# Kernel optimization log

Measured on AMD Instinct MI355X. Metric: run time of the kernel, lower is better.

The kernel has to match this reference:

```python
import jax, jax.numpy as jnp
import numpy as np
from jax import lax

B, Q, T, G = 128, 900, 256, 20
FOCAL_ALPHA, FOCAL_GAMMA = 0.25, 2.0
COEF_BBOX, COEF_GIOU, COEF_CLASS = 5.0, 2.0, 1.0
EPS = 1e-6


def setup_inputs() -> dict:
    key = jax.random.key(0)
    k1, k2, k3, k4, k5 = jax.random.split(key, 5)
    pred_logits = jax.random.normal(k1, (B, Q, T), dtype=jnp.float32)
    # pred boxes in cxcywh, valid-ish: centers in (0.2,0.8), w/h in (0.05,0.3)
    cxy_p = jax.random.uniform(k2, (B, Q, 2), minval=0.2, maxval=0.8)
    wh_p = jax.random.uniform(k3, (B, Q, 2), minval=0.05, maxval=0.3)
    pred_boxes = jnp.concatenate([cxy_p, wh_p], axis=-1).astype(jnp.float32)
    cxy_t = jax.random.uniform(k4, (B, G, 2), minval=0.2, maxval=0.8)
    wh_t = jax.random.uniform(k5, (B, G, 2), minval=0.05, maxval=0.3)
    tgt_boxes = jnp.concatenate([cxy_t, wh_t], axis=-1).astype(jnp.float32)
    ks, kl = jax.random.split(jax.random.fold_in(key, 7))
    start = jax.random.randint(ks, (B, G, 1), 0, T - 6)
    length = jax.random.randint(kl, (B, G, 1), 1, 6)
    tokens_positive = jnp.concatenate([start, start + length], axis=-1).astype(jnp.int32)
    return {"pred_logits": pred_logits, "pred_boxes": pred_boxes,
            "tgt_boxes": tgt_boxes, "tokens_positive": tokens_positive}


def cxcywh_to_xyxy(b):
    cx, cy, w, h = b[..., 0], b[..., 1], b[..., 2], b[..., 3]
    return jnp.stack([cx - 0.5 * w, cy - 0.5 * h, cx + 0.5 * w, cy + 0.5 * h], axis=-1)


def box_iou_pairwise(b1, b2):
    # b1: [Q,4], b2: [G,4] xyxy -> iou [Q,G]
    a1 = (b1[:, 2] - b1[:, 0]) * (b1[:, 3] - b1[:, 1])
    a2 = (b2[:, 2] - b2[:, 0]) * (b2[:, 3] - b2[:, 1])
    lt = jnp.maximum(b1[:, None, :2], b2[None, :, :2])
    rb = jnp.minimum(b1[:, None, 2:], b2[None, :, 2:])
    wh = jnp.clip(rb - lt, 0.0)
    inter = wh[..., 0] * wh[..., 1]
    union = a1[:, None] + a2[None, :] - inter
    return inter / union


def giou_elementwise(b1, b2):
    # b1, b2: [G,4] xyxy (matched pairs) -> giou [G]
    a1 = (b1[:, 2] - b1[:, 0]) * (b1[:, 3] - b1[:, 1])
    a2 = (b2[:, 2] - b2[:, 0]) * (b2[:, 3] - b2[:, 1])
    lt = jnp.maximum(b1[:, :2], b2[:, :2])
    rb = jnp.minimum(b1[:, 2:], b2[:, 2:])
    wh = jnp.clip(rb - lt, 0.0)
    inter = wh[:, 0] * wh[:, 1]
    union = a1 + a2 - inter
    iou = inter / union
    lt_c = jnp.minimum(b1[:, :2], b2[:, :2])
    rb_c = jnp.maximum(b1[:, 2:], b2[:, 2:])
    wh_c = jnp.clip(rb_c - lt_c, 0.0)
    area_c = wh_c[:, 0] * wh_c[:, 1]
    return iou - (area_c - union) / area_c


def ensure_valid_boxes(b):
    x1, y1, x2, y2 = b[:, 0], b[:, 1], b[:, 2], b[:, 3]
    x2v = jnp.maximum(x2, x1 + EPS)
    y2v = jnp.maximum(y2, y1 + EPS)
    return jnp.clip(jnp.stack([x1, y1, x2v, y2v], axis=-1), 0.0, 1.0)


def sigmoid_focal_loss(logits, targets):
    p = jax.nn.sigmoid(logits)
    ce = jnp.maximum(logits, 0.0) - logits * targets + jnp.log1p(jnp.exp(-jnp.abs(logits)))
    p_t = p * targets + (1.0 - p) * (1.0 - targets)
    loss = ce * (1.0 - p_t) ** FOCAL_GAMMA
    alpha_t = FOCAL_ALPHA * targets + (1.0 - FOCAL_ALPHA) * (1.0 - targets)
    return (alpha_t * loss).mean()


def _per_batch(pred_boxes_b, pred_logits_b, tgt_boxes_b, spans_b):
    pred_xyxy = cxcywh_to_xyxy(pred_boxes_b)          # [Q,4]
    tgt_xyxy = cxcywh_to_xyxy(tgt_boxes_b)            # [G,4]
    iou = lax.stop_gradient(box_iou_pairwise(pred_xyxy, tgt_xyxy))  # [Q,G]

    # greedy sequential matching: for each gt column, argmax over remaining preds
    def step(mat, g):
        best = jnp.argmax(mat[:, g])
        mat = mat.at[best].set(-1.0)
        return mat, best
    _, matched = lax.scan(step, iou, jnp.arange(G))   # [G] pred indices

    matched_boxes = pred_boxes_b[matched]             # [G,4]
    loss_bbox = jnp.sum(jnp.abs(matched_boxes - tgt_boxes_b))

    matched_xyxy = ensure_valid_boxes(cxcywh_to_xyxy(matched_boxes))
    tgt_valid = ensure_valid_boxes(tgt_xyxy)
    giou = giou_elementwise(matched_xyxy, tgt_valid)
    loss_giou = jnp.sum(1.0 - giou)

    # target_classes [Q,T]: rows at matched indices get 1 over the gt token span
    pos = jnp.arange(T)
    span_mask = ((pos[None, :] >= spans_b[:, 0:1]) & (pos[None, :] < spans_b[:, 1:2])).astype(jnp.float32)  # [G,T]
    target_classes = jnp.zeros((Q, T), dtype=jnp.float32).at[matched].max(span_mask)

    loss_class = sigmoid_focal_loss(pred_logits_b, target_classes)
    return loss_bbox, loss_giou, loss_class


def reference(pred_logits, pred_boxes, tgt_boxes, tokens_positive):
    lb, lg, lc = jax.vmap(_per_batch)(pred_boxes, pred_logits, tgt_boxes, tokens_positive)
    num_boxes = jnp.float32(B * G)
    loss_bbox = COEF_BBOX * jnp.sum(lb) / num_boxes
    loss_giou = COEF_GIOU * jnp.sum(lg) / num_boxes
    loss_class = COEF_CLASS * jnp.sum(lc) / num_boxes
    loss_total = loss_bbox + loss_giou + loss_class
    return jnp.stack([loss_bbox, loss_giou, loss_class, loss_total])
```

## Files before the change

kernel.cpp:

```cpp
#include <hip/hip_runtime.h>
#include <hip/hip_bf16.h>

#define NB 128
#define NQ 900
#define NT 256
#define NG 20
#define NR 15
#define FOCAL_BLOCKS 1800
#define MATCH_BLOCKS 128
#define TOTAL_BLOCKS (FOCAL_BLOCKS + MATCH_BLOCKS)
#define FWAVES (FOCAL_BLOCKS * 4)

#define WS_BB 7200
#define WS_GI 7328
#define WS_DL 7456

__device__ __forceinline__ float clamp01(float v) {
    return fminf(fmaxf(v, 0.0f), 1.0f);
}

__device__ __forceinline__ float focal_neg_term(float x) {
    float ax  = fabsf(x);
    float em  = __expf(-ax);
    float a1  = 1.0f + em;
    float ce  = fmaxf(x, 0.0f) + __logf(a1);
    float inv = __builtin_amdgcn_rcpf(a1);
    float p   = (x >= 0.0f) ? inv : em * inv;
    return ce * p * p;
}

__device__ __forceinline__ float focal_delta_term(float x) {
    float ax     = fabsf(x);
    float em     = __expf(-ax);
    float a1     = 1.0f + em;
    float lg     = __logf(a1);
    float ce0    = fmaxf(x, 0.0f) + lg;
    float ce1    = ce0 - x;
    float inv    = __builtin_amdgcn_rcpf(a1);
    float em_inv = em * inv;
    float p      = (x >= 0.0f) ? inv : em_inv;
    float omp    = (x >= 0.0f) ? em_inv : inv;
    return 0.25f * ce1 * omp * omp - 0.75f * ce0 * p * p;
}

__global__ __launch_bounds__(256, 8) void main_kernel(
    const float4* __restrict__ logits,
    const float4* __restrict__ pred_boxes,
    const float4* __restrict__ tgt_boxes,
    const int2*   __restrict__ tokens,
    float*        __restrict__ ws)
{
    __shared__ float4 sxy[904];
    __shared__ float  sar[904];

    if (blockIdx.x < MATCH_BLOCKS) {
        const int b   = blockIdx.x;
        const int tid = threadIdx.x;

        for (int q = tid; q < 904; q += 256) {
            float4 xy; float a;
            if (q < NQ) {
                float4 pb = pred_boxes[b * NQ + q];
                xy.x = pb.x - 0.5f * pb.z;
                xy.y = pb.y - 0.5f * pb.w;
                xy.z = pb.x + 0.5f * pb.z;
                xy.w = pb.y + 0.5f * pb.w;
                a = (xy.z - xy.x) * (xy.w - xy.y);
            } else {
                xy = make_float4(2.0f, 2.0f, 2.0f, 2.0f);
                a  = 1.0f;
            }
            sxy[q] = xy;
            sar[q] = a;
        }
        __syncthreads();
        if (tid >= 64) return;
        const int lane = tid;

        int avail = (lane < 4) ? 0x7fff : 0x3fff;
        int my_q = 0;

        for (int g = 0; g < NG; ++g) {
            float4 tb = tgt_boxes[b * NG + g];
            float gx1 = tb.x - 0.5f * tb.z, gy1 = tb.y - 0.5f * tb.w;
            float gx2 = tb.x + 0.5f * tb.z, gy2 = tb.y + 0.5f * tb.w;
            float ga  = (gx2 - gx1) * (gy2 - gy1);
            float bv = -2.0f;
            int   bi = 0x7fffffff;
            #pragma unroll 5
            for (int r = 0; r < NR; ++r) {
                int q = lane + 64 * r;
                float4 p  = sxy[q];
                float  pa = sar[q];
                float ix1 = fmaxf(p.x, gx1), iy1 = fmaxf(p.y, gy1);
                float ix2 = fminf(p.z, gx2), iy2 = fminf(p.w, gy2);
                float iw = fmaxf(ix2 - ix1, 0.0f), ih = fmaxf(iy2 - iy1, 0.0f);
                float inter = iw * ih;
                float v = inter / (pa + ga - inter);
                bool ok = (avail >> r) & 1;
                v = ok ? v : -1.0f;
                if (v > bv) { bv = v; bi = q; }
            }
            #pragma unroll
            for (int off = 1; off < 64; off <<= 1) {
                float ov = __shfl_xor(bv, off);
                int   oi = __shfl_xor(bi, off);
                if (ov > bv || (ov == bv && oi < bi)) { bv = ov; bi = oi; }
            }
            if (lane == g) my_q = bi;
            if ((bi & 63) == lane) avail &= ~(1 << (bi >> 6));
        }

        float lb = 0.0f, lgi = 0.0f, dl = 0.0f;
        if (lane < NG) {
            int g = lane, q = my_q;
            float4 pb = pred_boxes[b * NQ + q];
            float4 tb = tgt_boxes[b * NG + g];
            lb = fabsf(pb.x - tb.x) + fabsf(pb.y - tb.y) +
                 fabsf(pb.z - tb.z) + fabsf(pb.w - tb.w);

            float mx1 = pb.x - 0.5f * pb.z, my1 = pb.y - 0.5f * pb.w;
            float mx2 = pb.x + 0.5f * pb.z, my2 = pb.y + 0.5f * pb.w;
            mx2 = fmaxf(mx2, mx1 + 1e-6f);  my2 = fmaxf(my2, my1 + 1e-6f);
            mx1 = clamp01(mx1); my1 = clamp01(my1);
            mx2 = clamp01(mx2); my2 = clamp01(my2);

            float gx1 = tb.x - 0.5f * tb.z, gy1 = tb.y - 0.5f * tb.w;
            float gx2 = tb.x + 0.5f * tb.z, gy2 = tb.y + 0.5f * tb.w;
            gx2 = fmaxf(gx2, gx1 + 1e-6f);  gy2 = fmaxf(gy2, gy1 + 1e-6f);
            gx1 = clamp01(gx1); gy1 = clamp01(gy1);
            gx2 = clamp01(gx2); gy2 = clamp01(gy2);

            float a1 = (mx2 - mx1) * (my2 - my1);
            float a2 = (gx2 - gx1) * (gy2 - gy1);
            float ix1 = fmaxf(mx1, gx1), iy1 = fmaxf(my1, gy1);
            float ix2 = fminf(mx2, gx2), iy2 = fminf(my2, gy2);
            float iw = fmaxf(ix2 - ix1, 0.0f), ih = fmaxf(iy2 - iy1, 0.0f);
            float inter = iw * ih;
            float uni   = a1 + a2 - inter;
            float iou   = inter / uni;
            float cx1 = fminf(mx1, gx1), cy1 = fminf(my1, gy1);
            float cx2 = fmaxf(mx2, gx2), cy2 = fmaxf(my2, gy2);
            float ac  = fmaxf(cx2 - cx1, 0.0f) * fmaxf(cy2 - cy1, 0.0f);
            lgi = 1.0f - (iou - (ac - uni) / ac);

            int2 tk = tokens[b * NG + g];
            const float* rowp = (const float*)logits + (size_t)(b * NQ + q) * NT;
            for (int t = tk.x; t < tk.y; ++t) dl += focal_delta_term(rowp[t]);
        }
        #pragma unroll
        for (int off = 32; off > 0; off >>= 1) {
            lb  += __shfl_down(lb,  off);
            lgi += __shfl_down(lgi, off);
            dl  += __shfl_down(dl,  off);
        }
        if (lane == 0) {
            ws[WS_BB + b] = lb;
            ws[WS_GI + b] = lgi;
            ws[WS_DL + b] = dl;
        }
    } else {
        const int lane = threadIdx.x & 63;
        const int gw   = ((blockIdx.x - MATCH_BLOCKS) * 256 + threadIdx.x) >> 6;
        const float4* __restrict__ base = logits + lane;

        float sum = 0.0f;
        int row0 = gw * 4;
        float4 c0 = base[(size_t)(row0 + 0) * (NT / 4)];
        float4 c1 = base[(size_t)(row0 + 1) * (NT / 4)];
        float4 c2 = base[(size_t)(row0 + 2) * (NT / 4)];
        float4 c3 = base[(size_t)(row0 + 3) * (NT / 4)];
        #pragma unroll
        for (int i = 0; i < 4; ++i) {
            float4 n0, n1, n2, n3;
            if (i < 3) {
                int nr = (gw + (i + 1) * FWAVES) * 4;
                n0 = base[(size_t)(nr + 0) * (NT / 4)];
                n1 = base[(size_t)(nr + 1) * (NT / 4)];
                n2 = base[(size_t)(nr + 2) * (NT / 4)];
                n3 = base[(size_t)(nr + 3) * (NT / 4)];
            }
            sum += focal_neg_term(c0.x) + focal_neg_term(c0.y) +
                   focal_neg_term(c0.z) + focal_neg_term(c0.w);
            sum += focal_neg_term(c1.x) + focal_neg_term(c1.y) +
                   focal_neg_term(c1.z) + focal_neg_term(c1.w);
            sum += focal_neg_term(c2.x) + focal_neg_term(c2.y) +
                   focal_neg_term(c2.z) + focal_neg_term(c2.w);
            sum += focal_neg_term(c3.x) + focal_neg_term(c3.y) +
                   focal_neg_term(c3.z) + focal_neg_term(c3.w);
            if (i < 3) { c0 = n0; c1 = n1; c2 = n2; c3 = n3; }
        }
        #pragma unroll
        for (int off = 32; off > 0; off >>= 1) sum += __shfl_down(sum, off);
        if (lane == 0) ws[gw] = sum;
    }
}

__global__ __launch_bounds__(256) void finalize_kernel(
    const float* __restrict__ ws, float* __restrict__ out)
{
    const int tid  = threadIdx.x;
    const int lane = tid & 63;
    const int wav  = tid >> 6;

    float s_neg = 0.0f;
    for (int i = tid; i < FWAVES; i += 256) s_neg += ws[i];
    float s_bb = 0.0f, s_gi = 0.0f, s_dl = 0.0f;
    if (tid < NB) {
        s_bb = ws[WS_BB + tid];
        s_gi = ws[WS_GI + tid];
        s_dl = ws[WS_DL + tid];
    }
    #pragma unroll
    for (int off = 32; off > 0; off >>= 1) {
        s_neg += __shfl_down(s_neg, off);
        s_bb  += __shfl_down(s_bb,  off);
        s_gi  += __shfl_down(s_gi,  off);
        s_dl  += __shfl_down(s_dl,  off);
    }
    __shared__ float red[4][4];
    if (lane == 0) {
        red[0][wav] = s_neg; red[1][wav] = s_bb;
        red[2][wav] = s_gi;  red[3][wav] = s_dl;
    }
    __syncthreads();
    if (tid == 0) {
        float neg = red[0][0] + red[0][1] + red[0][2] + red[0][3];
        float bb  = red[1][0] + red[1][1] + red[1][2] + red[1][3];
        float gi  = red[2][0] + red[2][1] + red[2][2] + red[2][3];
        float dlt = red[3][0] + red[3][1] + red[3][2] + red[3][3];
        const float num_boxes = (float)(NB * NG);
        float lb = 5.0f * bb / num_boxes;
        float lg = 2.0f * gi / num_boxes;
        float cls_sum = 0.75f * neg + dlt;
        float lc = (cls_sum / (float)(NQ * NT)) / num_boxes;
        out[0] = lb;
        out[1] = lg;
        out[2] = lc;
        out[3] = lb + lg + lc;
    }
}

extern "C" void kernel_launch(void* const* d_in, const int* in_sizes, int n_in,
                              void* d_out, int out_size, void* d_ws, size_t ws_size,
                              hipStream_t stream) {
    const float4* pred_logits4 = (const float4*)d_in[0];
    const float4* pred_boxes4  = (const float4*)d_in[1];
    const float4* tgt_boxes4   = (const float4*)d_in[2];
    const int2*   tokens2      = (const int2*)d_in[3];

    float* ws = (float*)d_ws;

    main_kernel<<<TOTAL_BLOCKS, 256, 0, stream>>>(pred_logits4, pred_boxes4,
                                                  tgt_boxes4, tokens2, ws);
    finalize_kernel<<<1, 256, 0, stream>>>(ws, (float*)d_out);
}
```

Baseline: 202.6 us.

## Spread greedy IoU matching across all four waves with register-held boxes

The matching phase no longer has one wave scan 900 queries from LDS. All 256 threads now keep up to four predicted boxes in registers, and each greedy step does a shuffle reduction per wave followed by a cross-wave reduction through shared memory. This removes the LDS staging and gives each thread a shorter serial scan per target. In exchange it adds two block barriers per target (40 in total), and dropping the occupancy hint in launch_bounds may change register allocation for the focal blocks.

```diff
diff --git a/kernel.cpp b/kernel.cpp
--- a/kernel.cpp
+++ b/kernel.cpp
@@ -5,7 +5,6 @@
 #define NQ 900
 #define NT 256
 #define NG 20
-#define NR 15
 #define FOCAL_BLOCKS 1800
 #define MATCH_BLOCKS 128
 #define TOTAL_BLOCKS (FOCAL_BLOCKS + MATCH_BLOCKS)
@@ -43,42 +42,38 @@
     return 0.25f * ce1 * omp * omp - 0.75f * ce0 * p * p;
 }
 
-__global__ __launch_bounds__(256, 8) void main_kernel(
+__global__ __launch_bounds__(256) void main_kernel(
     const float4* __restrict__ logits,
     const float4* __restrict__ pred_boxes,
     const float4* __restrict__ tgt_boxes,
     const int2*   __restrict__ tokens,
     float*        __restrict__ ws)
 {
-    __shared__ float4 sxy[904];
-    __shared__ float  sar[904];
+    __shared__ float s_bv[4];
+    __shared__ int   s_bi[4];
 
     if (blockIdx.x < MATCH_BLOCKS) {
-        const int b   = blockIdx.x;
-        const int tid = threadIdx.x;
-
-        for (int q = tid; q < 904; q += 256) {
-            float4 xy; float a;
+        const int b    = blockIdx.x;
+        const int tid  = threadIdx.x;
+        const int lane = tid & 63;
+        const int wav  = tid >> 6;
+
+        float px1[4], py1[4], px2[4], py2[4], pa[4];
+        #pragma unroll
+        for (int r = 0; r < 4; ++r) {
+            int q = tid + 256 * r;
             if (q < NQ) {
                 float4 pb = pred_boxes[b * NQ + q];
-                xy.x = pb.x - 0.5f * pb.z;
-                xy.y = pb.y - 0.5f * pb.w;
-                xy.z = pb.x + 0.5f * pb.z;
-                xy.w = pb.y + 0.5f * pb.w;
-                a = (xy.z - xy.x) * (xy.w - xy.y);
+                px1[r] = pb.x - 0.5f * pb.z; py1[r] = pb.y - 0.5f * pb.w;
+                px2[r] = pb.x + 0.5f * pb.z; py2[r] = pb.y + 0.5f * pb.w;
+                pa[r]  = (px2[r] - px1[r]) * (py2[r] - py1[r]);
             } else {
-                xy = make_float4(2.0f, 2.0f, 2.0f, 2.0f);
-                a  = 1.0f;
-            }
-            sxy[q] = xy;
-            sar[q] = a;
-        }
-        __syncthreads();
-        if (tid >= 64) return;
-        const int lane = tid;
-
-        int avail = (lane < 4) ? 0x7fff : 0x3fff;
-        int my_q = 0;
+                px1[r] = 2.0f; py1[r] = 2.0f; px2[r] = 2.0f; py2[r] = 2.0f;
+                pa[r]  = 1.0f;
+            }
+        }
+        int avail = (tid < 132) ? 0xF : 0x7;
+        int my_q  = 0;
 
         for (int g = 0; g < NG; ++g) {
             float4 tb = tgt_boxes[b * NG + g];
@@ -87,18 +82,16 @@
             float ga  = (gx2 - gx1) * (gy2 - gy1);
             float bv = -2.0f;
             int   bi = 0x7fffffff;
-            #pragma unroll 5
-            for (int r = 0; r < NR; ++r) {
-                int q = lane + 64 * r;
-                float4 p  = sxy[q];
-                float  pa = sar[q];
-                float ix1 = fmaxf(p.x, gx1), iy1 = fmaxf(p.y, gy1);
-                float ix2 = fminf(p.z, gx2), iy2 = fminf(p.w, gy2);
+            #pragma unroll
+            for (int r = 0; r < 4; ++r) {
+                float ix1 = fmaxf(px1[r], gx1), iy1 = fmaxf(py1[r], gy1);
+                float ix2 = fminf(px2[r], gx2), iy2 = fminf(py2[r], gy2);
                 float iw = fmaxf(ix2 - ix1, 0.0f), ih = fmaxf(iy2 - iy1, 0.0f);
                 float inter = iw * ih;
-                float v = inter / (pa + ga - inter);
+                float v = inter / (pa[r] + ga - inter);
                 bool ok = (avail >> r) & 1;
                 v = ok ? v : -1.0f;
+                int q = tid + 256 * r;
                 if (v > bv) { bv = v; bi = q; }
             }
             #pragma unroll
@@ -107,9 +100,20 @@
                 int   oi = __shfl_xor(bi, off);
                 if (ov > bv || (ov == bv && oi < bi)) { bv = ov; bi = oi; }
             }
-            if (lane == g) my_q = bi;
-            if ((bi & 63) == lane) avail &= ~(1 << (bi >> 6));
-        }
+            if (lane == 0) { s_bv[wav] = bv; s_bi[wav] = bi; }
+            __syncthreads();
+            float wbv = s_bv[0]; int wbi = s_bi[0];
+            #pragma unroll
+            for (int w = 1; w < 4; ++w) {
+                float ov = s_bv[w]; int oi = s_bi[w];
+                if (ov > wbv || (ov == wbv && oi < wbi)) { wbv = ov; wbi = oi; }
+            }
+            __syncthreads();
+            if (tid == g) my_q = wbi;
+            if ((wbi & 255) == tid) avail &= ~(1 << (wbi >> 8));
+        }
+
+        if (tid >= 64) return;
 
         float lb = 0.0f, lgi = 0.0f, dl = 0.0f;
         if (lane < NG) {
```

After: 187.3 us. 1.08x faster.
